# Optimization experiments

Measured on AMD Instinct MI355X. Metric: run time of the kernel, lower is better.

Reference implementation:

```python
import jax, jax.numpy as jnp
import numpy as np

N_NODES = 100000
DEGREE = 16
FEAT = 128
HID = 64
OUT = 16
BATCH = 4096
K = 12  # n_neibs


def setup_inputs() -> dict:
    key = jax.random.key(0)
    ks = jax.random.split(key, 12)
    idx0 = jax.random.randint(ks[0], (BATCH,), 0, N_NODES, dtype=jnp.int64 if jax.config.jax_enable_x64 else jnp.int32)
    buf1 = jax.random.randint(ks[1], (BATCH, K), 0, 1000000)
    buf2 = jax.random.randint(ks[2], (BATCH * K, K), 0, 1000000)
    indptr = jnp.arange(N_NODES) * DEGREE            # CSR row pointers (fixed degree)
    indices = jax.random.randint(ks[3], (N_NODES * DEGREE,), 0, N_NODES)
    degrees = jnp.full((N_NODES,), DEGREE, dtype=jnp.int32)
    emb_weight = jax.random.normal(ks[4], (N_NODES, FEAT), dtype=jnp.float32)
    enc_w = jax.random.normal(ks[5], (HID, FEAT), dtype=jnp.float32) * (1.0 / np.sqrt(FEAT))
    h1_w = jax.random.normal(ks[6], (HID, 2 * HID), dtype=jnp.float32) * (1.0 / np.sqrt(2 * HID))
    h1_b = jnp.zeros((HID,), jnp.float32)
    h2_w = jax.random.normal(ks[7], (HID, HID), dtype=jnp.float32) * (1.0 / np.sqrt(HID))
    h2_b = jnp.zeros((HID,), jnp.float32)
    out_w = jax.random.normal(ks[8], (OUT, HID), dtype=jnp.float32) * (1.0 / np.sqrt(HID))
    out_b = jnp.zeros((OUT,), jnp.float32)
    return dict(idx0=idx0, buf1=buf1, buf2=buf2, indptr=indptr, indices=indices,
                degrees=degrees, emb_weight=emb_weight, enc_w=enc_w,
                h1_w=h1_w, h1_b=h1_b, h2_w=h2_w, h2_b=h2_b, out_w=out_w, out_b=out_b)


def _sample_neighbors(nodes, buf, indptr, indices, degrees):
    # nodes: [M], buf: [M, K] random ints -> neighbor node ids [M, K]
    neibs = buf % degrees[nodes][:, None]
    offsets = indptr[nodes][:, None] + neibs
    return indices[offsets]


def reference(idx0, buf1, buf2, indptr, indices, degrees, emb_weight,
              enc_w, h1_w, h1_b, h2_w, h2_b, out_w, out_b):
    B = idx0.shape[0]
    idx1 = _sample_neighbors(idx0, buf1, indptr, indices, degrees)              # [B, K]
    idx2 = _sample_neighbors(idx1.reshape(B * K), buf2, indptr, indices, degrees)
    idx2 = idx2.reshape(B, K, K)                                                # [B, K, K]

    enc_1hop = jax.nn.relu(jnp.einsum('bkf,hf->bkh', emb_weight[idx1], enc_w))  # [B, K, H]
    enc_2hop = jax.nn.relu(jnp.einsum('bkjf,hf->bkjh', emb_weight[idx2], enc_w))
    avg_2hop = enc_2hop.mean(axis=-2)                                           # [B, K, H]

    h1 = jnp.concatenate([enc_1hop, avg_2hop], axis=-1)                         # [B, K, 2H]
    h1 = jax.nn.relu(jnp.einsum('bkc,hc->bkh', h1, h1_w) + h1_b)
    avg_1hop = h1.mean(axis=-2)                                                 # [B, H]
    h0 = jax.nn.relu(avg_1hop @ h2_w.T + h2_b)
    return h0 @ out_w.T + out_b                                                 # [B, OUT]
```

## Files before the change

### kernel.cpp

```cpp
#include <hip/hip_runtime.h>

#define NNODES 100000

typedef __attribute__((ext_vector_type(8))) short bf16x8;
typedef __attribute__((ext_vector_type(4))) float floatx4;

union PackU { uint4 u; bf16x8 v; };

__device__ __forceinline__ uint pack_hi2(float x0, float x1) {
    return (__float_as_uint(x1) & 0xFFFF0000u) | (__float_as_uint(x0) >> 16);
}
__device__ __forceinline__ uint pack_lo2(float x0, float x1) {
    float l0 = x0 - __uint_as_float(__float_as_uint(x0) & 0xFFFF0000u);
    float l1 = x1 - __uint_as_float(__float_as_uint(x1) & 0xFFFF0000u);
    return (__float_as_uint(l1) & 0xFFFF0000u) | (__float_as_uint(l0) >> 16);
}
__device__ __forceinline__ ushort bf_rne(float x) {
    unsigned u = __float_as_uint(x);
    return (ushort)((u + 0x7FFFu + ((u >> 16) & 1u)) >> 16);
}
__device__ __forceinline__ float lo16f(uint u) { return __uint_as_float(u << 16); }
__device__ __forceinline__ float hi16f(uint u) { return __uint_as_float(u & 0xFFFF0000u); }

__global__ __launch_bounds__(256) void k_gemm(const float* __restrict__ emb,
                                              const float* __restrict__ enc_w,
                                              const float* __restrict__ h1_w,
                                              ushort* __restrict__ encAB) {
    __shared__ ushort smem[35840];
    ushort* sB_h = smem;
    ushort* sB_l = smem + 8704;
    ushort* sW_h = smem + 17408;
    ushort* sW_l = smem + 26624;
    ushort* sE_h = smem;
    ushort* sE_l = smem + 4608;

    const int t = threadIdx.x;
    const int n0 = blockIdx.x * 64;
    const int w = t >> 6, lane = t & 63;
    const int m = lane & 15, q = lane >> 4;

    int nn = n0 + w * 16 + m; if (nn > NNODES - 1) nn = NNODES - 1;
    const float* rowp = emb + (size_t)nn * 128 + q * 8;
    bf16x8 a_h[4], a_l[4];
#pragma unroll
    for (int ks = 0; ks < 4; ++ks) {
        float4 f0 = *(const float4*)(rowp + ks * 32);
        float4 f1 = *(const float4*)(rowp + ks * 32 + 4);
        PackU ph, pl;
        ph.u = (uint4){pack_hi2(f0.x, f0.y), pack_hi2(f0.z, f0.w),
                       pack_hi2(f1.x, f1.y), pack_hi2(f1.z, f1.w)};
        pl.u = (uint4){pack_lo2(f0.x, f0.y), pack_lo2(f0.z, f0.w),
                       pack_lo2(f1.x, f1.y), pack_lo2(f1.z, f1.w)};
        a_h[ks] = ph.v; a_l[ks] = pl.v;
    }

#pragma unroll
    for (int r = 0; r < 8; ++r) {
        int c4 = (t + 256 * r) * 4;
        int h = c4 >> 7, f = c4 & 127;
        float4 v = *(const float4*)&enc_w[c4];
        *(uint2*)&sB_h[h * 136 + f] = (uint2){pack_hi2(v.x, v.y), pack_hi2(v.z, v.w)};
        *(uint2*)&sB_l[h * 136 + f] = (uint2){pack_lo2(v.x, v.y), pack_lo2(v.z, v.w)};
    }
#pragma unroll
    for (int r = 0; r < 8; ++r) {
        int c4 = (t + 256 * r) * 4;
        int o = c4 >> 7, cc = c4 & 127;
        int o2 = o + (cc & 64), col = cc & 63;
        float4 v = *(const float4*)&h1_w[c4];
        *(uint2*)&sW_h[o2 * 72 + col] = (uint2){pack_hi2(v.x, v.y), pack_hi2(v.z, v.w)};
        *(uint2*)&sW_l[o2 * 72 + col] = (uint2){pack_lo2(v.x, v.y), pack_lo2(v.z, v.w)};
    }
    __syncthreads();

    floatx4 acc[4] = {};
#pragma unroll
    for (int ht = 0; ht < 4; ++ht) {
        const ushort* pBh = &sB_h[(ht * 16 + m) * 136 + q * 8];
#pragma unroll
        for (int ks = 0; ks < 4; ++ks) {
            bf16x8 bh = *(const bf16x8*)(pBh + ks * 32);
            bf16x8 bl = *(const bf16x8*)(pBh + 8704 + ks * 32);
            acc[ht] = __builtin_amdgcn_mfma_f32_16x16x32_bf16(a_h[ks], bh, acc[ht], 0, 0, 0);
            acc[ht] = __builtin_amdgcn_mfma_f32_16x16x32_bf16(a_l[ks], bh, acc[ht], 0, 0, 0);
            acc[ht] = __builtin_amdgcn_mfma_f32_16x16x32_bf16(a_h[ks], bl, acc[ht], 0, 0, 0);
        }
    }
    __syncthreads();

#pragma unroll
    for (int ht = 0; ht < 4; ++ht)
#pragma unroll
        for (int i = 0; i < 4; ++i) {
            float v = fmaxf(acc[ht][i], 0.f);
            int row = w * 16 + q * 4 + i, col = ht * 16 + m;
            uint uv = __float_as_uint(v);
            sE_h[row * 72 + col] = (ushort)(uv >> 16);
            float lo = v - __uint_as_float(uv & 0xFFFF0000u);
            sE_l[row * 72 + col] = (ushort)(__float_as_uint(lo) >> 16);
        }
    __syncthreads();

    bf16x8 e_h[2], e_l[2];
    {
        const ushort* pE = &sE_h[(w * 16 + m) * 72 + q * 8];
#pragma unroll
        for (int ks = 0; ks < 2; ++ks) {
            e_h[ks] = *(const bf16x8*)(pE + ks * 32);
            e_l[ks] = *(const bf16x8*)(pE + 4608 + ks * 32);
        }
    }
    floatx4 acc2[8] = {};
#pragma unroll
    for (int ot = 0; ot < 8; ++ot) {
        const ushort* pWh = &sW_h[(ot * 16 + m) * 72 + q * 8];
#pragma unroll
        for (int ks = 0; ks < 2; ++ks) {
            bf16x8 bh = *(const bf16x8*)(pWh + ks * 32);
            bf16x8 bl = *(const bf16x8*)(pWh + 9216 + ks * 32);
            acc2[ot] = __builtin_amdgcn_mfma_f32_16x16x32_bf16(e_h[ks], bh, acc2[ot], 0, 0, 0);
            acc2[ot] = __builtin_amdgcn_mfma_f32_16x16x32_bf16(e_l[ks], bh, acc2[ot], 0, 0, 0);
            acc2[ot] = __builtin_amdgcn_mfma_f32_16x16x32_bf16(e_h[ks], bl, acc2[ot], 0, 0, 0);
        }
    }
#pragma unroll
    for (int ot = 0; ot < 8; ++ot)
#pragma unroll
        for (int i = 0; i < 4; ++i) {
            int n = n0 + w * 16 + q * 4 + i;
            if (n < NNODES) encAB[n * 128 + ot * 16 + m] = bf_rne(acc2[ot][i]);
        }
}

__global__ __launch_bounds__(256) void k_gather_head(const int* __restrict__ idx0,
                                                     const int* __restrict__ buf1,
                                                     const int* __restrict__ buf2,
                                                     const int* __restrict__ indices,
                                                     const ushort* __restrict__ encAB,
                                                     const float* __restrict__ h1_b,
                                                     const float* __restrict__ h2_w,
                                                     const float* __restrict__ h2_b,
                                                     const float* __restrict__ out_w,
                                                     const float* __restrict__ out_b,
                                                     float* __restrict__ out) {
    __shared__ int s_idx1[48];
    __shared__ int s_idx2[576];
    __shared__ float sW2[64 * 65];
    __shared__ float sWo[64 * 17];
    __shared__ float sAvg[4][64];
    __shared__ float sH0[4][64];

    const int t = threadIdx.x;
    const int b0 = blockIdx.x * 4;

    if (t < 48) {
        int bl = t / 12;
        s_idx1[t] = indices[idx0[b0 + bl] * 16 + (buf1[b0 * 12 + t] & 15)];
    }
#pragma unroll
    for (int r = 0; r < 16; ++r) {
        int e = t + 256 * r;
        sW2[(e & 63) * 65 + (e >> 6)] = h2_w[e];
    }
#pragma unroll
    for (int r = 0; r < 4; ++r) {
        int e = t + 256 * r;
        sWo[(e & 63) * 17 + (e >> 6)] = out_w[e];
    }
    __syncthreads();

#pragma unroll
    for (int r = 0; r < 3; ++r) {
        int s = t + 256 * r;
        if (s < 576) {
            int bk = s / 12;
            s_idx2[s] = indices[s_idx1[bk] * 16 + (buf2[b0 * 144 + s] & 15)];
        }
    }
    __syncthreads();

    const int w = t >> 6, lane = t & 63;
    const int pp = lane >> 5, c = lane & 31;
    const uint* __restrict__ encAB32 = (const uint*)encAB;
    const int* myi1 = &s_idx1[w * 12];
    const int* myi2 = &s_idx2[w * 144];
    float2 bb = *(const float2*)&h1_b[2 * c];
    float hs0 = 0.f, hs1 = 0.f;
#pragma unroll 3
    for (int k = 0; k < 12; ++k) {
        uint av = encAB32[myi1[k] * 64 + c];
        float s0 = 0.f, s1 = 0.f;
#pragma unroll
        for (int jj = 0; jj < 6; ++jj) {
            uint v = encAB32[myi2[k * 12 + 2 * jj + pp] * 64 + 32 + c];
            s0 += lo16f(v); s1 += hi16f(v);
        }
        s0 += __shfl_xor(s0, 32);
        s1 += __shfl_xor(s1, 32);
        hs0 += fmaxf(lo16f(av) + s0 * (1.f / 12.f) + bb.x, 0.f);
        hs1 += fmaxf(hi16f(av) + s1 * (1.f / 12.f) + bb.y, 0.f);
    }
    if (pp == 0) {
        sAvg[w][2 * c]     = hs0 * (1.f / 12.f);
        sAvg[w][2 * c + 1] = hs1 * (1.f / 12.f);
    }
    __syncthreads();

    {
        float acc = h2_b[lane];
#pragma unroll 8
        for (int i = 0; i < 64; ++i)
            acc += sAvg[w][i] * sW2[i * 65 + lane];
        sH0[w][lane] = fmaxf(acc, 0.f);
    }
    __syncthreads();
    if (t < 64) {
        int g2 = t >> 4, o = t & 15;
        float acc2 = out_b[o];
#pragma unroll 8
        for (int i = 0; i < 64; ++i)
            acc2 += sH0[g2][i] * sWo[i * 17 + o];
        out[(b0 + g2) * 16 + o] = acc2;
    }
}

extern "C" void kernel_launch(void* const* d_in, const int* in_sizes, int n_in,
                              void* d_out, int out_size, void* d_ws, size_t ws_size,
                              hipStream_t stream) {
    const int*   idx0    = (const int*)d_in[0];
    const int*   buf1    = (const int*)d_in[1];
    const int*   buf2    = (const int*)d_in[2];
    const int*   indices = (const int*)d_in[4];
    const float* emb     = (const float*)d_in[6];
    const float* enc_w   = (const float*)d_in[7];
    const float* h1_w    = (const float*)d_in[8];
    const float* h1_b    = (const float*)d_in[9];
    const float* h2_w    = (const float*)d_in[10];
    const float* h2_b    = (const float*)d_in[11];
    const float* out_w   = (const float*)d_in[12];
    const float* out_b   = (const float*)d_in[13];
    (void)d_in[3]; (void)d_in[5];
    float* out = (float*)d_out;

    ushort* encAB = (ushort*)d_ws;

    k_gemm<<<1563, 256, 0, stream>>>(emb, enc_w, h1_w, encAB);
    k_gather_head<<<1024, 256, 0, stream>>>(idx0, buf1, buf2, indices, encAB,
                                            h1_b, h2_w, h2_b, out_w, out_b, out);
}
```

Measured before the change: 147.0 us.

## Widen gather loads to uint2 and double-buffer neighbor chunks in gather head

The gather loop now gives each lane 8-byte loads covering four bf16 features, with four row groups of 16 lanes reducing 2-hop sums through two xor shuffles. Neighbor rows are fetched in chunks of three hops into two register buffers, so the loads for the next chunk are issued before the current one is consumed. The aim is more memory-level parallelism and fewer load instructions in the latency-bound random gather. In exchange it uses more registers and adds an extra shuffle stage per hop.

Result: slower. 153.3 us (+4.3%).

```diff
diff --git a/kernel.cpp b/kernel.cpp
--- a/kernel.cpp
+++ b/kernel.cpp
@@ -130,6 +130,51 @@
             int n = n0 + w * 16 + q * 4 + i;
             if (n < NNODES) encAB[n * 128 + ot * 16 + m] = bf_rne(acc2[ot][i]);
         }
+}
+
+struct Chunk3 { uint2 vB[3][3]; uint2 vA[3]; };
+
+__device__ __forceinline__ void chunk_load(Chunk3& c, const uint* __restrict__ encAB32,
+                                           const int* __restrict__ myi1,
+                                           const int* __restrict__ myi2,
+                                           int kc, int rg, int cg) {
+    int rA[3], rB[3][3];
+#pragma unroll
+    for (int k3 = 0; k3 < 3; ++k3) {
+        int k = kc * 3 + k3;
+        rA[k3] = myi1[k];
+#pragma unroll
+        for (int jj = 0; jj < 3; ++jj) rB[k3][jj] = myi2[k * 12 + rg + 4 * jj];
+    }
+#pragma unroll
+    for (int k3 = 0; k3 < 3; ++k3) {
+#pragma unroll
+        for (int jj = 0; jj < 3; ++jj)
+            c.vB[k3][jj] = *(const uint2*)&encAB32[rB[k3][jj] * 64 + 32 + 2 * cg];
+        c.vA[k3] = *(const uint2*)&encAB32[rA[k3] * 64 + 2 * cg];
+    }
+}
+
+__device__ __forceinline__ void chunk_consume(Chunk3& c, float (&hs)[4], const float4& bb) {
+#pragma unroll
+    for (int k3 = 0; k3 < 3; ++k3) {
+        float s0 = 0.f, s1 = 0.f, s2 = 0.f, s3 = 0.f;
+#pragma unroll
+        for (int jj = 0; jj < 3; ++jj) {
+            uint2 v = c.vB[k3][jj];
+            s0 += lo16f(v.x); s1 += hi16f(v.x);
+            s2 += lo16f(v.y); s3 += hi16f(v.y);
+        }
+        s0 += __shfl_xor(s0, 16); s0 += __shfl_xor(s0, 32);
+        s1 += __shfl_xor(s1, 16); s1 += __shfl_xor(s1, 32);
+        s2 += __shfl_xor(s2, 16); s2 += __shfl_xor(s2, 32);
+        s3 += __shfl_xor(s3, 16); s3 += __shfl_xor(s3, 32);
+        uint2 a = c.vA[k3];
+        hs[0] += fmaxf(lo16f(a.x) + s0 * (1.f / 12.f) + bb.x, 0.f);
+        hs[1] += fmaxf(hi16f(a.x) + s1 * (1.f / 12.f) + bb.y, 0.f);
+        hs[2] += fmaxf(lo16f(a.y) + s2 * (1.f / 12.f) + bb.z, 0.f);
+        hs[3] += fmaxf(hi16f(a.y) + s3 * (1.f / 12.f) + bb.w, 0.f);
+    }
 }
 
 __global__ __launch_bounds__(256) void k_gather_head(const int* __restrict__ idx0,
@@ -180,29 +225,30 @@
     __syncthreads();
 
     const int w = t >> 6, lane = t & 63;
-    const int pp = lane >> 5, c = lane & 31;
+    const int rg = lane >> 4, cg = lane & 15;
     const uint* __restrict__ encAB32 = (const uint*)encAB;
     const int* myi1 = &s_idx1[w * 12];
     const int* myi2 = &s_idx2[w * 144];
-    float2 bb = *(const float2*)&h1_b[2 * c];
-    float hs0 = 0.f, hs1 = 0.f;
-#pragma unroll 3
-    for (int k = 0; k < 12; ++k) {
-        uint av = encAB32[myi1[k] * 64 + c];
-        float s0 = 0.f, s1 = 0.f;
-#pragma unroll
-        for (int jj = 0; jj < 6; ++jj) {
-            uint v = encAB32[myi2[k * 12 + 2 * jj + pp] * 64 + 32 + c];
-            s0 += lo16f(v); s1 += hi16f(v);
-        }
-        s0 += __shfl_xor(s0, 32);
-        s1 += __shfl_xor(s1, 32);
-        hs0 += fmaxf(lo16f(av) + s0 * (1.f / 12.f) + bb.x, 0.f);
-        hs1 += fmaxf(hi16f(av) + s1 * (1.f / 12.f) + bb.y, 0.f);
-    }
-    if (pp == 0) {
-        sAvg[w][2 * c]     = hs0 * (1.f / 12.f);
-        sAvg[w][2 * c + 1] = hs1 * (1.f / 12.f);
+    float4 bb = *(const float4*)&h1_b[4 * cg];
+    float hs[4] = {0.f, 0.f, 0.f, 0.f};
+
+    Chunk3 c0, c1;
+    chunk_load(c0, encAB32, myi1, myi2, 0, rg, cg);
+    chunk_load(c1, encAB32, myi1, myi2, 1, rg, cg);
+    chunk_consume(c0, hs, bb);
+    chunk_load(c0, encAB32, myi1, myi2, 2, rg, cg);
+    chunk_consume(c1, hs, bb);
+    chunk_load(c1, encAB32, myi1, myi2, 3, rg, cg);
+    chunk_consume(c0, hs, bb);
+    chunk_consume(c1, hs, bb);
+
+    if (rg == 0) {
+        float4 av;
+        av.x = hs[0] * (1.f / 12.f);
+        av.y = hs[1] * (1.f / 12.f);
+        av.z = hs[2] * (1.f / 12.f);
+        av.w = hs[3] * (1.f / 12.f);
+        *(float4*)&sAvg[w][4 * cg] = av;
     }
     __syncthreads();
 
```

## Pre-pack weight MFMA fragments once in a prep kernel, read from global

Applied to the files above, without the earlier changes.

Adds a single-block prep kernel that converts enc_w and h1_w into hi/lo bf16 split fragments already in MFMA lane order, stored in workspace. The GEMM kernel no longer converts and stages the weights in LDS in every block; it loads the fragments straight from global/L2. This shrinks shared memory to just the activation tile, and launch_bounds(256,4) asks for higher occupancy. The cost is an extra kernel launch and uncached-in-LDS global reads of weights per wave, which rely on L2 hits.

Result: slower. 151.4 us (+3.0%).

```diff
diff --git a/kernel.cpp b/kernel.cpp
--- a/kernel.cpp
+++ b/kernel.cpp
@@ -22,18 +22,46 @@
 __device__ __forceinline__ float lo16f(uint u) { return __uint_as_float(u << 16); }
 __device__ __forceinline__ float hi16f(uint u) { return __uint_as_float(u & 0xFFFF0000u); }
 
-__global__ __launch_bounds__(256) void k_gemm(const float* __restrict__ emb,
-                                              const float* __restrict__ enc_w,
+__global__ __launch_bounds__(256) void k_prep(const float* __restrict__ enc_w,
                                               const float* __restrict__ h1_w,
-                                              ushort* __restrict__ encAB) {
-    __shared__ ushort smem[35840];
-    ushort* sB_h = smem;
-    ushort* sB_l = smem + 8704;
-    ushort* sW_h = smem + 17408;
-    ushort* sW_l = smem + 26624;
-    ushort* sE_h = smem;
-    ushort* sE_l = smem + 4608;
-
+                                              uint4* __restrict__ frgB,
+                                              uint4* __restrict__ frgW) {
+    const int t = threadIdx.x;
+#pragma unroll
+    for (int r = 0; r < 8; ++r) {
+        int id = t + 256 * r;
+        int lane = id & 63, m = lane & 15, q = lane >> 4;
+        if (id < 1024) {
+            int ks = (id >> 6) & 3, ht = id >> 8;
+            const float* p = enc_w + (ht * 16 + m) * 128 + ks * 32 + q * 8;
+            float4 f0 = *(const float4*)p, f1 = *(const float4*)(p + 4);
+            frgB[((ht * 4 + ks) * 2 + 0) * 64 + lane] =
+                (uint4){pack_hi2(f0.x, f0.y), pack_hi2(f0.z, f0.w),
+                        pack_hi2(f1.x, f1.y), pack_hi2(f1.z, f1.w)};
+            frgB[((ht * 4 + ks) * 2 + 1) * 64 + lane] =
+                (uint4){pack_lo2(f0.x, f0.y), pack_lo2(f0.z, f0.w),
+                        pack_lo2(f1.x, f1.y), pack_lo2(f1.z, f1.w)};
+        } else {
+            int id2 = id - 1024;
+            int ks = (id2 >> 6) & 1, ot = id2 >> 7;
+            int o2 = ot * 16 + m;
+            const float* p = h1_w + (o2 & 63) * 128 + (o2 & 64) + ks * 32 + q * 8;
+            float4 f0 = *(const float4*)p, f1 = *(const float4*)(p + 4);
+            frgW[((ot * 2 + ks) * 2 + 0) * 64 + lane] =
+                (uint4){pack_hi2(f0.x, f0.y), pack_hi2(f0.z, f0.w),
+                        pack_hi2(f1.x, f1.y), pack_hi2(f1.z, f1.w)};
+            frgW[((ot * 2 + ks) * 2 + 1) * 64 + lane] =
+                (uint4){pack_lo2(f0.x, f0.y), pack_lo2(f0.z, f0.w),
+                        pack_lo2(f1.x, f1.y), pack_lo2(f1.z, f1.w)};
+        }
+    }
+}
+
+__global__ __launch_bounds__(256, 4) void k_gemm(const float* __restrict__ emb,
+                                                 const uint4* __restrict__ frgB,
+                                                 const uint4* __restrict__ frgW,
+                                                 ushort* __restrict__ encAB) {
+    __shared__ ushort sE[2 * 64 * 72];
     const int t = threadIdx.x;
     const int n0 = blockIdx.x * 64;
     const int w = t >> 6, lane = t & 63;
@@ -54,39 +82,20 @@
         a_h[ks] = ph.v; a_l[ks] = pl.v;
     }
 
-#pragma unroll
-    for (int r = 0; r < 8; ++r) {
-        int c4 = (t + 256 * r) * 4;
-        int h = c4 >> 7, f = c4 & 127;
-        float4 v = *(const float4*)&enc_w[c4];
-        *(uint2*)&sB_h[h * 136 + f] = (uint2){pack_hi2(v.x, v.y), pack_hi2(v.z, v.w)};
-        *(uint2*)&sB_l[h * 136 + f] = (uint2){pack_lo2(v.x, v.y), pack_lo2(v.z, v.w)};
-    }
-#pragma unroll
-    for (int r = 0; r < 8; ++r) {
-        int c4 = (t + 256 * r) * 4;
-        int o = c4 >> 7, cc = c4 & 127;
-        int o2 = o + (cc & 64), col = cc & 63;
-        float4 v = *(const float4*)&h1_w[c4];
-        *(uint2*)&sW_h[o2 * 72 + col] = (uint2){pack_hi2(v.x, v.y), pack_hi2(v.z, v.w)};
-        *(uint2*)&sW_l[o2 * 72 + col] = (uint2){pack_lo2(v.x, v.y), pack_lo2(v.z, v.w)};
-    }
-    __syncthreads();
-
+    const uint4* pB = frgB + lane;
     floatx4 acc[4] = {};
 #pragma unroll
     for (int ht = 0; ht < 4; ++ht) {
-        const ushort* pBh = &sB_h[(ht * 16 + m) * 136 + q * 8];
 #pragma unroll
         for (int ks = 0; ks < 4; ++ks) {
-            bf16x8 bh = *(const bf16x8*)(pBh + ks * 32);
-            bf16x8 bl = *(const bf16x8*)(pBh + 8704 + ks * 32);
-            acc[ht] = __builtin_amdgcn_mfma_f32_16x16x32_bf16(a_h[ks], bh, acc[ht], 0, 0, 0);
-            acc[ht] = __builtin_amdgcn_mfma_f32_16x16x32_bf16(a_l[ks], bh, acc[ht], 0, 0, 0);
-            acc[ht] = __builtin_amdgcn_mfma_f32_16x16x32_bf16(a_h[ks], bl, acc[ht], 0, 0, 0);
-        }
-    }
-    __syncthreads();
+            PackU bh, bl;
+            bh.u = pB[((ht * 4 + ks) * 2 + 0) * 64];
+            bl.u = pB[((ht * 4 + ks) * 2 + 1) * 64];
+            acc[ht] = __builtin_amdgcn_mfma_f32_16x16x32_bf16(a_h[ks], bh.v, acc[ht], 0, 0, 0);
+            acc[ht] = __builtin_amdgcn_mfma_f32_16x16x32_bf16(a_l[ks], bh.v, acc[ht], 0, 0, 0);
+            acc[ht] = __builtin_amdgcn_mfma_f32_16x16x32_bf16(a_h[ks], bl.v, acc[ht], 0, 0, 0);
+        }
+    }
 
 #pragma unroll
     for (int ht = 0; ht < 4; ++ht)
@@ -95,32 +104,33 @@
             float v = fmaxf(acc[ht][i], 0.f);
             int row = w * 16 + q * 4 + i, col = ht * 16 + m;
             uint uv = __float_as_uint(v);
-            sE_h[row * 72 + col] = (ushort)(uv >> 16);
+            sE[row * 72 + col] = (ushort)(uv >> 16);
             float lo = v - __uint_as_float(uv & 0xFFFF0000u);
-            sE_l[row * 72 + col] = (ushort)(__float_as_uint(lo) >> 16);
+            sE[64 * 72 + row * 72 + col] = (ushort)(__float_as_uint(lo) >> 16);
         }
     __syncthreads();
 
     bf16x8 e_h[2], e_l[2];
     {
-        const ushort* pE = &sE_h[(w * 16 + m) * 72 + q * 8];
+        const ushort* pE = sE + (w * 16 + m) * 72 + q * 8;
 #pragma unroll
         for (int ks = 0; ks < 2; ++ks) {
             e_h[ks] = *(const bf16x8*)(pE + ks * 32);
-            e_l[ks] = *(const bf16x8*)(pE + 4608 + ks * 32);
-        }
-    }
+            e_l[ks] = *(const bf16x8*)(pE + 64 * 72 + ks * 32);
+        }
+    }
+    const uint4* pW = frgW + lane;
     floatx4 acc2[8] = {};
 #pragma unroll
     for (int ot = 0; ot < 8; ++ot) {
-        const ushort* pWh = &sW_h[(ot * 16 + m) * 72 + q * 8];
 #pragma unroll
         for (int ks = 0; ks < 2; ++ks) {
-            bf16x8 bh = *(const bf16x8*)(pWh + ks * 32);
-            bf16x8 bl = *(const bf16x8*)(pWh + 9216 + ks * 32);
-            acc2[ot] = __builtin_amdgcn_mfma_f32_16x16x32_bf16(e_h[ks], bh, acc2[ot], 0, 0, 0);
-            acc2[ot] = __builtin_amdgcn_mfma_f32_16x16x32_bf16(e_l[ks], bh, acc2[ot], 0, 0, 0);
-            acc2[ot] = __builtin_amdgcn_mfma_f32_16x16x32_bf16(e_h[ks], bl, acc2[ot], 0, 0, 0);
+            PackU wh, wl;
+            wh.u = pW[((ot * 2 + ks) * 2 + 0) * 64];
+            wl.u = pW[((ot * 2 + ks) * 2 + 1) * 64];
+            acc2[ot] = __builtin_amdgcn_mfma_f32_16x16x32_bf16(e_h[ks], wh.v, acc2[ot], 0, 0, 0);
+            acc2[ot] = __builtin_amdgcn_mfma_f32_16x16x32_bf16(e_l[ks], wh.v, acc2[ot], 0, 0, 0);
+            acc2[ot] = __builtin_amdgcn_mfma_f32_16x16x32_bf16(e_h[ks], wl.v, acc2[ot], 0, 0, 0);
         }
     }
 #pragma unroll
@@ -243,8 +253,11 @@
     float* out = (float*)d_out;
 
     ushort* encAB = (ushort*)d_ws;
-
-    k_gemm<<<1563, 256, 0, stream>>>(emb, enc_w, h1_w, encAB);
+    uint4* frgB = (uint4*)((char*)d_ws + 25600000);
+    uint4* frgW = frgB + 2048;
+
+    k_prep<<<1, 256, 0, stream>>>(enc_w, h1_w, frgB, frgW);
+    k_gemm<<<1563, 256, 0, stream>>>(emb, frgB, frgW, encAB);
     k_gather_head<<<1024, 256, 0, stream>>>(idx0, buf1, buf2, indices, encAB,
                                             h1_b, h2_w, h2_b, out_w, out_b, out);
 }
```
